# Optimization experiments

Hardware: AMD Instinct MI355X
Metric: run time of the kernel (lower is better)

## Reference

```python
import jax, jax.numpy as jnp
import numpy as np

B, S, D = 4, 2048, 1024
E, H, TOP_K = 8, 4096, 2


def setup_inputs() -> dict:
    key = jax.random.key(0)
    ks = jax.random.split(key, 5)
    scale = 0.02
    return {
        "x": jax.random.normal(ks[0], (B, S, D), dtype=jnp.float32),
        "Wr": jax.random.normal(ks[1], (D, E), dtype=jnp.float32) * scale,
        "br": jnp.zeros((E,), dtype=jnp.float32),
        "W1": jax.random.normal(ks[2], (E, D, H), dtype=jnp.float32) * scale,
        "b1": jnp.zeros((E, H), dtype=jnp.float32),
        "W2": jax.random.normal(ks[3], (E, H, D), dtype=jnp.float32) * scale,
        "b2": jnp.zeros((E, D), dtype=jnp.float32),
    }


def reference(x, Wr, br, W1, b1, W2, b2):
    b, s, d = x.shape
    xf = x.reshape(-1, d)                                   # [T, D]
    gate = jax.nn.softmax(xf @ Wr + br, axis=-1)            # [T, E]
    top_w, top_i = jax.lax.top_k(gate, TOP_K)               # [T, K]
    top_w = top_w / jnp.sum(top_w, axis=-1, keepdims=True)
    # combine[t, e] = sum_i top_w[t, i] * 1{top_i[t, i] == e}
    combine = jnp.sum(jax.nn.one_hot(top_i, E, dtype=xf.dtype) * top_w[..., None], axis=1)  # [T, E]
    # Dense all-expert FFN (same math as the masked per-expert loops in torch)
    h = jax.nn.gelu(jnp.einsum('td,edh->teh', xf, W1) + b1, approximate=False)  # [T, E, H]
    out = jnp.einsum('teh,ehd,te->td', h, W2, combine) + combine @ b2           # [T, D]
    return out.reshape(b, s, d)
```

## Files before the change

kernel.cpp:

```cpp
#include <hip/hip_runtime.h>
#include <cstdio>


#define T_TOK 8192
#define DIM   1024
#define NEXP  8
#define HID   4096
#define MAXR  17408

typedef float          f32x4   __attribute__((ext_vector_type(4)));
typedef short          bf16x8  __attribute__((ext_vector_type(8)));
typedef unsigned short u16x8   __attribute__((ext_vector_type(8)));
typedef unsigned short u16x4   __attribute__((ext_vector_type(4)));

static __device__ __forceinline__ unsigned short f2bf(float f) {
  unsigned int u = __builtin_bit_cast(unsigned int, f);
  u = (u + 0x7FFFu + ((u >> 16) & 1u)) >> 16;
  return (unsigned short)u;
}

static __device__ __forceinline__ void gl16(const void* g, void* l) {
  __builtin_amdgcn_global_load_lds(
      (const __attribute__((address_space(1))) unsigned int*)g,
      (__attribute__((address_space(3))) unsigned int*)l,
      16, 0, 0);
}

__global__ __launch_bounds__(256) void router_k(const float* __restrict__ x,
                                                const float* __restrict__ Wr,
                                                const float* __restrict__ br,
                                                int* __restrict__ meta,
                                                int2* __restrict__ top_i,
                                                float2* __restrict__ top_w) {
  int lane = threadIdx.x & 63;
  int wid  = threadIdx.x >> 6;
  int t = blockIdx.x * 4 + wid;
  const float* xp = x + (size_t)t * DIM + lane * 16;
  float acc[NEXP];
#pragma unroll
  for (int e = 0; e < NEXP; ++e) acc[e] = 0.f;
#pragma unroll
  for (int j = 0; j < 16; j += 4) {
    float4 xv = *(const float4*)(xp + j);
    const float* wp = Wr + (size_t)(lane * 16 + j) * NEXP;
#pragma unroll
    for (int jj = 0; jj < 4; ++jj) {
      float xs = jj == 0 ? xv.x : jj == 1 ? xv.y : jj == 2 ? xv.z : xv.w;
      float4 w0 = *(const float4*)(wp + jj * NEXP);
      float4 w1 = *(const float4*)(wp + jj * NEXP + 4);
      acc[0] += xs * w0.x; acc[1] += xs * w0.y; acc[2] += xs * w0.z; acc[3] += xs * w0.w;
      acc[4] += xs * w1.x; acc[5] += xs * w1.y; acc[6] += xs * w1.z; acc[7] += xs * w1.w;
    }
  }
#pragma unroll
  for (int off = 32; off > 0; off >>= 1) {
#pragma unroll
    for (int e = 0; e < NEXP; ++e) acc[e] += __shfl_xor(acc[e], off);
  }
  if (lane == 0) {
    float l[NEXP];
#pragma unroll
    for (int e = 0; e < NEXP; ++e) l[e] = acc[e] + br[e];
    int e1 = 0;
#pragma unroll
    for (int e = 1; e < NEXP; ++e) if (l[e] > l[e1]) e1 = e;
    int e2 = (e1 == 0) ? 1 : 0;
#pragma unroll
    for (int e = 0; e < NEXP; ++e) if (e != e1 && l[e] > l[e2]) e2 = e;
    float g  = expf(l[e2] - l[e1]);
    float w1 = 1.f / (1.f + g);
    top_i[t] = make_int2(e1, e2);
    top_w[t] = make_float2(w1, 1.f - w1);
    atomicAdd(&meta[e1], 1);
    atomicAdd(&meta[e2], 1);
  }
}

__global__ void prefix_k(int* __restrict__ meta) {
  if (threadIdx.x == 0) {
    int s = 0;
#pragma unroll
    for (int e = 0; e < NEXP; ++e) {
      meta[16 + e] = s;
      s += (meta[e] + 127) & ~127;
    }
    meta[24] = s;
    meta[25] = s;
  }
}

__global__ __launch_bounds__(256) void fill_k(int* __restrict__ tok_of_row,
                                              float* __restrict__ wt_of_row) {
  int i = blockIdx.x * 256 + threadIdx.x;
  if (i < MAXR) { tok_of_row[i] = 0; wt_of_row[i] = 0.f; }
}

__global__ __launch_bounds__(256) void scatter_k(const int2* __restrict__ top_i,
                                                 const float2* __restrict__ top_w,
                                                 int* __restrict__ meta,
                                                 int* __restrict__ row_of,
                                                 int* __restrict__ tok_of_row,
                                                 float* __restrict__ wt_of_row) {
  int t = blockIdx.x * 256 + threadIdx.x;
  int2  ei = top_i[t];
  float2 w = top_w[t];
  int p = atomicAdd(&meta[8 + ei.x], 1);
  int r = meta[16 + ei.x] + p;
  tok_of_row[r] = t; wt_of_row[r] = w.x; row_of[t * 2] = r;
  p = atomicAdd(&meta[8 + ei.y], 1);
  r = meta[16 + ei.y] + p;
  tok_of_row[r] = t; wt_of_row[r] = w.y; row_of[t * 2 + 1] = r;
}

__global__ __launch_bounds__(256) void gather_k(const float* __restrict__ x,
                                                const int* __restrict__ tok_of_row,
                                                const int* __restrict__ meta,
                                                unsigned short* __restrict__ xg) {
  int r = blockIdx.x;
  if (r >= meta[25]) return;
  int t = tok_of_row[r];
  int c = threadIdx.x * 4;
  float4 v = *(const float4*)(x + (size_t)t * DIM + c);
  u16x4 o;
  o[0] = f2bf(v.x); o[1] = f2bf(v.y); o[2] = f2bf(v.z); o[3] = f2bf(v.w);
  *(u16x4*)(xg + (size_t)r * DIM + c) = o;
}

__global__ __launch_bounds__(256) void transpose_convert_k(const float* __restrict__ W,
                                                           unsigned short* __restrict__ WT,
                                                           int R, int C) {
  __shared__ float tile[32][33];
  int e = blockIdx.z;
  int c0 = blockIdx.x * 32, r0 = blockIdx.y * 32;
  const float* Wp = W + (size_t)e * R * C;
  unsigned short* Op = WT + (size_t)e * R * C;
  int tr = threadIdx.x >> 3;
  int tc = (threadIdx.x & 7) * 4;
  float4 v = *(const float4*)(Wp + (size_t)(r0 + tr) * C + c0 + tc);
  tile[tr][tc] = v.x; tile[tr][tc + 1] = v.y; tile[tr][tc + 2] = v.z; tile[tr][tc + 3] = v.w;
  __syncthreads();
  int oc  = threadIdx.x >> 3;
  int orr = (threadIdx.x & 7) * 4;
  u16x4 o;
#pragma unroll
  for (int j = 0; j < 4; ++j) o[j] = f2bf(tile[orr + j][oc]);
  *(u16x4*)(Op + (size_t)(c0 + oc) * R + r0 + orr) = o;
}

template <int KTOT, int NTOT, int EPI>
__global__ __launch_bounds__(256) void gemm_k(const unsigned short* __restrict__ A,
                                              const unsigned short* __restrict__ Bt,
                                              const float* __restrict__ bias,
                                              const int* __restrict__ meta,
                                              const float* __restrict__ wt_of_row,
                                              void* __restrict__ Cout) {
  constexpr int NXB = MAXR / 128;
  constexpr int NWG = NXB * (NTOT / 128);
  int id = (blockIdx.x & 7) * (NWG / 8) + (blockIdx.x >> 3);
  int row0 = (id % NXB) * 128;
  int n0   = (id / NXB) * 128;
  if (row0 >= meta[25]) return;
  int e = 0;
  while (meta[17 + e] <= row0) ++e;
  const unsigned short* Bp = Bt + (size_t)e * NTOT * KTOT;

  __shared__ __align__(16) unsigned short Ash[128 * 32];
  __shared__ __align__(16) unsigned short Bsh[128 * 32];

  int tid = threadIdx.x;
  int lane = tid & 63, wid = tid >> 6;
  int wm = wid >> 1, wn = wid & 1;
  int rs = tid >> 2;
  int cs = (tid & 3) * 8;

  const unsigned short* Ag = A  + (size_t)(row0 + rs) * KTOT + cs;
  const unsigned short* Bg = Bp + (size_t)(n0   + rs) * KTOT + cs;
  unsigned short* Al = Ash + tid * 8;
  unsigned short* Bl = Bsh + tid * 8;

  f32x4 acc[4][4];
#pragma unroll
  for (int i = 0; i < 4; ++i)
#pragma unroll
    for (int j = 0; j < 4; ++j) acc[i][j] = (f32x4){0.f, 0.f, 0.f, 0.f};

  int am = lane & 15, ak = (lane >> 4) * 8;

  for (int kt = 0; kt < KTOT; kt += 32) {
    __syncthreads();
    gl16(Ag + kt, Al);
    gl16(Ag + 64 * KTOT + kt, Al + 2048);
    gl16(Bg + kt, Bl);
    gl16(Bg + 64 * KTOT + kt, Bl + 2048);
    __syncthreads();
    bf16x8 af[4], bfr[4];
#pragma unroll
    for (int i = 0; i < 4; ++i)
      af[i] = *(const bf16x8*)(Ash + (wm * 64 + i * 16 + am) * 32 + ak);
#pragma unroll
    for (int j = 0; j < 4; ++j)
      bfr[j] = *(const bf16x8*)(Bsh + (wn * 64 + j * 16 + am) * 32 + ak);
#pragma unroll
    for (int i = 0; i < 4; ++i)
#pragma unroll
      for (int j = 0; j < 4; ++j)
        acc[i][j] = __builtin_amdgcn_mfma_f32_16x16x32_bf16(af[i], bfr[j], acc[i][j], 0, 0, 0);
  }

  int rbase = row0 + wm * 64 + (lane >> 4) * 4;
  int nbase = n0 + wn * 64 + (lane & 15);
  if constexpr (EPI == 0) {
    unsigned short* Hp = (unsigned short*)Cout;
    const float* bp = bias + (size_t)e * NTOT;
#pragma unroll
    for (int i = 0; i < 4; ++i) {
#pragma unroll
      for (int j = 0; j < 4; ++j) {
        int n = nbase + j * 16;
        float bv = bp[n];
#pragma unroll
        for (int rg = 0; rg < 4; ++rg) {
          int m = rbase + i * 16 + rg;
          float v = acc[i][j][rg] + bv;
          v = 0.5f * v * (1.f + erff(v * 0.70710678118654752f));
          Hp[(size_t)m * NTOT + n] = f2bf(v);
        }
      }
    }
  } else {
    float* Yp = (float*)Cout;
    const float* bp = bias + (size_t)e * NTOT;
#pragma unroll
    for (int i = 0; i < 4; ++i) {
#pragma unroll
      for (int rg = 0; rg < 4; ++rg) {
        int m = rbase + i * 16 + rg;
        float wt = wt_of_row[m];
#pragma unroll
        for (int j = 0; j < 4; ++j) {
          int n = nbase + j * 16;
          Yp[(size_t)m * NTOT + n] = (acc[i][j][rg] + bp[n]) * wt;
        }
      }
    }
  }
}

__global__ __launch_bounds__(256) void combine_k(const float* __restrict__ y,
                                                 const int* __restrict__ row_of,
                                                 float* __restrict__ out) {
  int t = blockIdx.x;
  int r0 = row_of[t * 2], r1 = row_of[t * 2 + 1];
  int c = threadIdx.x * 4;
  float4 a = *(const float4*)(y + (size_t)r0 * DIM + c);
  float4 b = *(const float4*)(y + (size_t)r1 * DIM + c);
  *(float4*)(out + (size_t)t * DIM + c) =
      make_float4(a.x + b.x, a.y + b.y, a.z + b.z, a.w + b.w);
}

extern "C" void kernel_launch(void* const* d_in, const int* in_sizes, int n_in,
                              void* d_out, int out_size, void* d_ws, size_t ws_size,
                              hipStream_t stream) {
  const float* x  = (const float*)d_in[0];
  const float* Wr = (const float*)d_in[1];
  const float* br = (const float*)d_in[2];
  const float* W1 = (const float*)d_in[3];
  const float* b1 = (const float*)d_in[4];
  const float* W2 = (const float*)d_in[5];
  const float* b2 = (const float*)d_in[6];
  float* out = (float*)d_out;

  char* base = (char*)d_ws;
  size_t off = 0;
  auto carve = [&](size_t bytes) -> void* {
    void* r = base + off;
    off = (off + bytes + 255) & ~(size_t)255;
    return r;
  };
  int*            meta       = (int*)carve(26 * 4);
  int2*           top_i      = (int2*)carve((size_t)T_TOK * 8);
  float2*         top_w      = (float2*)carve((size_t)T_TOK * 8);
  int*            row_of     = (int*)carve((size_t)T_TOK * 2 * 4);
  int*            tok_of_row = (int*)carve((size_t)MAXR * 4);
  float*          wt_of_row  = (float*)carve((size_t)MAXR * 4);
  unsigned short* xg         = (unsigned short*)carve((size_t)MAXR * DIM * 2);
  unsigned short* W1bT       = (unsigned short*)carve((size_t)NEXP * DIM * HID * 2);
  unsigned short* W2bT       = (unsigned short*)carve((size_t)NEXP * DIM * HID * 2);
  unsigned short* hbuf       = (unsigned short*)carve((size_t)MAXR * HID * 2);
  float*          ybuf       = (float*)carve((size_t)MAXR * DIM * 4);
  if (off > ws_size) {
    fprintf(stderr, "kernel_launch: ws_size too small: need %zu have %zu\n", off, ws_size);
    return;
  }

  hipMemsetAsync(meta, 0, 26 * 4, stream);
  hipLaunchKernelGGL(transpose_convert_k, dim3(HID / 32, DIM / 32, NEXP), dim3(256), 0, stream,
                     W1, W1bT, DIM, HID);
  hipLaunchKernelGGL(transpose_convert_k, dim3(DIM / 32, HID / 32, NEXP), dim3(256), 0, stream,
                     W2, W2bT, HID, DIM);
  hipLaunchKernelGGL(fill_k, dim3((MAXR + 255) / 256), dim3(256), 0, stream,
                     tok_of_row, wt_of_row);
  hipLaunchKernelGGL(router_k, dim3(T_TOK / 4), dim3(256), 0, stream,
                     x, Wr, br, meta, top_i, top_w);
  hipLaunchKernelGGL(prefix_k, dim3(1), dim3(64), 0, stream, meta);
  hipLaunchKernelGGL(scatter_k, dim3(T_TOK / 256), dim3(256), 0, stream,
                     top_i, top_w, meta, row_of, tok_of_row, wt_of_row);
  hipLaunchKernelGGL(gather_k, dim3(MAXR), dim3(256), 0, stream, x, tok_of_row, meta, xg);
  hipLaunchKernelGGL((gemm_k<DIM, HID, 0>), dim3(MAXR / 128 * (HID / 128)), dim3(256), 0, stream,
                     xg, W1bT, b1, meta, wt_of_row, (void*)hbuf);
  hipLaunchKernelGGL((gemm_k<HID, DIM, 1>), dim3(MAXR / 128 * (DIM / 128)), dim3(256), 0, stream,
                     hbuf, W2bT, b2, meta, wt_of_row, (void*)ybuf);
  hipLaunchKernelGGL(combine_k, dim3(T_TOK), dim3(256), 0, stream, ybuf, row_of, out);
}
```

Measured before the change: 893.7 us.

## Use 256x256 double-buffered swizzled GEMM tiles and atomic scatter-combine into output

Replaces the 128x128 single-buffered GEMM with a 512-thread 256x256 tile kernel. It double-buffers LDS in K-halves with interleaved barrier phases and an XOR swizzle to avoid bank conflicts, and raises MFMA priority with setprio. Expert row padding grows to 256 to match the larger tiles. The second GEMM now atomically adds weighted results straight into the zeroed output, which removes the ybuf round trip and the combine kernel. The cost is larger padding waste, float atomics to global memory, and 128 KB of LDS per workgroup.

Result: slower. 952.5 us (+6.6%).

```diff
diff --git a/kernel.cpp b/kernel.cpp
--- a/kernel.cpp
+++ b/kernel.cpp
@@ -6,11 +6,10 @@
 #define DIM   1024
 #define NEXP  8
 #define HID   4096
-#define MAXR  17408
+#define MAXR  18432
 
 typedef float          f32x4   __attribute__((ext_vector_type(4)));
 typedef short          bf16x8  __attribute__((ext_vector_type(8)));
-typedef unsigned short u16x8   __attribute__((ext_vector_type(8)));
 typedef unsigned short u16x4   __attribute__((ext_vector_type(4)));
 
 static __device__ __forceinline__ unsigned short f2bf(float f) {
@@ -25,6 +24,8 @@
       (__attribute__((address_space(3))) unsigned int*)l,
       16, 0, 0);
 }
+
+#define FENCE() asm volatile("" ::: "memory")
 
 __global__ __launch_bounds__(256) void router_k(const float* __restrict__ x,
                                                 const float* __restrict__ Wr,
@@ -82,7 +83,7 @@
 #pragma unroll
     for (int e = 0; e < NEXP; ++e) {
       meta[16 + e] = s;
-      s += (meta[e] + 127) & ~127;
+      s += (meta[e] + 255) & ~255;
     }
     meta[24] = s;
     meta[25] = s;
@@ -147,115 +148,150 @@
   *(u16x4*)(Op + (size_t)(c0 + oc) * R + r0 + orr) = o;
 }
 
+
+template <int KH, int MH>
+__device__ __forceinline__ void do_phase(const unsigned short* lds_, int buf,
+                                         int aoff, int boff, f32x4 (&acc)[8][4]) {
+  const unsigned short* Ar = lds_ + (buf * 4 + KH) * 8192 + aoff + MH * 2048;
+  const unsigned short* Br = lds_ + (buf * 4 + 2 + KH) * 8192 + boff;
+  bf16x8 af[4], bv[4];
+#pragma unroll
+  for (int r = 0; r < 4; ++r) af[r] = *(const bf16x8*)(Ar + r * 512);
+#pragma unroll
+  for (int n = 0; n < 4; ++n) bv[n] = *(const bf16x8*)(Br + n * 512);
+  __builtin_amdgcn_s_setprio(1);
+#pragma unroll
+  for (int r = 0; r < 4; ++r)
+#pragma unroll
+    for (int n = 0; n < 4; ++n)
+      acc[MH * 4 + r][n] =
+          __builtin_amdgcn_mfma_f32_16x16x32_bf16(af[r], bv[n], acc[MH * 4 + r][n], 0, 0, 0);
+  __builtin_amdgcn_s_setprio(0);
+}
+
 template <int KTOT, int NTOT, int EPI>
-__global__ __launch_bounds__(256) void gemm_k(const unsigned short* __restrict__ A,
-                                              const unsigned short* __restrict__ Bt,
-                                              const float* __restrict__ bias,
-                                              const int* __restrict__ meta,
-                                              const float* __restrict__ wt_of_row,
-                                              void* __restrict__ Cout) {
-  constexpr int NXB = MAXR / 128;
-  constexpr int NWG = NXB * (NTOT / 128);
-  int id = (blockIdx.x & 7) * (NWG / 8) + (blockIdx.x >> 3);
-  int row0 = (id % NXB) * 128;
-  int n0   = (id / NXB) * 128;
+__global__ __launch_bounds__(512, 2) void gemm8_k(const unsigned short* __restrict__ A,
+                                                  const unsigned short* __restrict__ Bt,
+                                                  const float* __restrict__ bias,
+                                                  const int* __restrict__ meta,
+                                                  const float* __restrict__ wt_of_row,
+                                                  const int* __restrict__ tok_of_row,
+                                                  void* __restrict__ Cout) {
+  constexpr int NTILES = NTOT / 256;
+  constexpr int NWG = (MAXR / 256) * NTILES;
+  constexpr int NT = KTOT / 64;
+  __shared__ __align__(16) unsigned short lds[65536];
+
+  int id = ((int)blockIdx.x & 7) * (NWG / 8) + ((int)blockIdx.x >> 3);
+  int row0 = (id / NTILES) * 256;
+  int n0   = (id % NTILES) * 256;
   if (row0 >= meta[25]) return;
   int e = 0;
   while (meta[17 + e] <= row0) ++e;
   const unsigned short* Bp = Bt + (size_t)e * NTOT * KTOT;
 
-  __shared__ __align__(16) unsigned short Ash[128 * 32];
-  __shared__ __align__(16) unsigned short Bsh[128 * 32];
-
   int tid = threadIdx.x;
   int lane = tid & 63, wid = tid >> 6;
-  int wm = wid >> 1, wn = wid & 1;
-  int rs = tid >> 2;
-  int cs = (tid & 3) * 8;
-
-  const unsigned short* Ag = A  + (size_t)(row0 + rs) * KTOT + cs;
-  const unsigned short* Bg = Bp + (size_t)(n0   + rs) * KTOT + cs;
-  unsigned short* Al = Ash + tid * 8;
-  unsigned short* Bl = Bsh + tid * 8;
-
-  f32x4 acc[4][4];
-#pragma unroll
-  for (int i = 0; i < 4; ++i)
-#pragma unroll
-    for (int j = 0; j < 4; ++j) acc[i][j] = (f32x4){0.f, 0.f, 0.f, 0.f};
-
-  int am = lane & 15, ak = (lane >> 4) * 8;
-
-  for (int kt = 0; kt < KTOT; kt += 32) {
-    __syncthreads();
-    gl16(Ag + kt, Al);
-    gl16(Ag + 64 * KTOT + kt, Al + 2048);
-    gl16(Bg + kt, Bl);
-    gl16(Bg + 64 * KTOT + kt, Bl + 2048);
-    __syncthreads();
-    bf16x8 af[4], bfr[4];
-#pragma unroll
-    for (int i = 0; i < 4; ++i)
-      af[i] = *(const bf16x8*)(Ash + (wm * 64 + i * 16 + am) * 32 + ak);
-#pragma unroll
-    for (int j = 0; j < 4; ++j)
-      bfr[j] = *(const bf16x8*)(Bsh + (wn * 64 + j * 16 + am) * 32 + ak);
-#pragma unroll
-    for (int i = 0; i < 4; ++i)
-#pragma unroll
-      for (int j = 0; j < 4; ++j)
-        acc[i][j] = __builtin_amdgcn_mfma_f32_16x16x32_bf16(af[i], bfr[j], acc[i][j], 0, 0, 0);
-  }
-
-  int rbase = row0 + wm * 64 + (lane >> 4) * 4;
-  int nbase = n0 + wn * 64 + (lane & 15);
+  int wm = wid >> 2, wn = wid & 3;
+
+  int r0s = tid >> 2, r1s = 128 + (tid >> 2);
+  int s0 = (tid & 3) ^ ((r0s >> 1) & 3);
+  int s1 = (tid & 3) ^ ((r1s >> 1) & 3);
+  const unsigned short* pA0 = A + (size_t)(row0 + r0s) * KTOT + s0 * 8;
+  const unsigned short* pA1 = A + (size_t)(row0 + r1s) * KTOT + s1 * 8;
+  const unsigned short* pB0 = Bp + (size_t)(n0 + r0s) * KTOT + s0 * 8;
+  const unsigned short* pB1 = Bp + (size_t)(n0 + r1s) * KTOT + s1 * 8;
+  int ldst = wid * 512;
+
+  auto stage = [&](int bufx, int mat, int kh, int kt) {
+    int rb = (bufx * 4 + mat * 2 + kh) * 8192 + ldst;
+    int ko = kt * 64 + kh * 32;
+    gl16((mat ? pB0 : pA0) + ko, (void*)(lds + rb));
+    gl16((mat ? pB1 : pA1) + ko, (void*)(lds + rb + 4096));
+  };
+
+  int sF = ((lane >> 4) ^ ((lane >> 1) & 3)) * 8;
+  int aoff = wm * 4096 + (lane & 15) * 32 + sF;
+  int boff = wn * 2048 + (lane & 15) * 32 + sF;
+
+  f32x4 acc[8][4];
+#pragma unroll
+  for (int r = 0; r < 8; ++r)
+#pragma unroll
+    for (int n = 0; n < 4; ++n) acc[r][n] = (f32x4){0.f, 0.f, 0.f, 0.f};
+
+  stage(0, 1, 0, 0); stage(0, 0, 0, 0); stage(0, 1, 1, 0); stage(0, 0, 1, 0);
+  FENCE();
+
+  for (int t = 0; t < NT - 1; ++t) {
+    int buf = t & 1, nb = buf ^ 1;
+    stage(nb, 1, 0, t + 1);
+    asm volatile("s_waitcnt vmcnt(6)" ::: "memory");
+    __builtin_amdgcn_s_barrier(); FENCE();
+    do_phase<0, 0>(lds, buf, aoff, boff, acc);
+    stage(nb, 0, 0, t + 1); FENCE();
+    __builtin_amdgcn_s_barrier(); FENCE();
+    do_phase<0, 1>(lds, buf, aoff, boff, acc);
+    stage(nb, 1, 1, t + 1);
+    asm volatile("s_waitcnt vmcnt(6)" ::: "memory");
+    __builtin_amdgcn_s_barrier(); FENCE();
+    do_phase<1, 0>(lds, buf, aoff, boff, acc);
+    stage(nb, 0, 1, t + 1); FENCE();
+    __builtin_amdgcn_s_barrier(); FENCE();
+    do_phase<1, 1>(lds, buf, aoff, boff, acc);
+  }
+  {
+    int buf = (NT - 1) & 1;
+    asm volatile("s_waitcnt vmcnt(4)" ::: "memory");
+    __builtin_amdgcn_s_barrier(); FENCE();
+    do_phase<0, 0>(lds, buf, aoff, boff, acc);
+    __builtin_amdgcn_s_barrier(); FENCE();
+    do_phase<0, 1>(lds, buf, aoff, boff, acc);
+    asm volatile("s_waitcnt vmcnt(0)" ::: "memory");
+    __builtin_amdgcn_s_barrier(); FENCE();
+    do_phase<1, 0>(lds, buf, aoff, boff, acc);
+    __builtin_amdgcn_s_barrier(); FENCE();
+    do_phase<1, 1>(lds, buf, aoff, boff, acc);
+  }
+
+  int rb2 = row0 + wm * 128 + ((lane >> 4) << 2);
+  int nb2 = n0 + wn * 64 + (lane & 15);
   if constexpr (EPI == 0) {
     unsigned short* Hp = (unsigned short*)Cout;
     const float* bp = bias + (size_t)e * NTOT;
 #pragma unroll
-    for (int i = 0; i < 4; ++i) {
-#pragma unroll
-      for (int j = 0; j < 4; ++j) {
-        int n = nbase + j * 16;
-        float bv = bp[n];
-#pragma unroll
-        for (int rg = 0; rg < 4; ++rg) {
-          int m = rbase + i * 16 + rg;
-          float v = acc[i][j][rg] + bv;
+    for (int r = 0; r < 8; ++r)
+#pragma unroll
+      for (int n = 0; n < 4; ++n) {
+        int ncol = nb2 + n * 16;
+        float bv = bp[ncol];
+#pragma unroll
+        for (int g = 0; g < 4; ++g) {
+          int m = rb2 + r * 16 + g;
+          float v = acc[r][n][g] + bv;
           v = 0.5f * v * (1.f + erff(v * 0.70710678118654752f));
-          Hp[(size_t)m * NTOT + n] = f2bf(v);
+          Hp[(size_t)m * NTOT + ncol] = f2bf(v);
         }
       }
-    }
   } else {
-    float* Yp = (float*)Cout;
+    float* Op = (float*)Cout;
     const float* bp = bias + (size_t)e * NTOT;
 #pragma unroll
-    for (int i = 0; i < 4; ++i) {
-#pragma unroll
-      for (int rg = 0; rg < 4; ++rg) {
-        int m = rbase + i * 16 + rg;
+    for (int r = 0; r < 8; ++r)
+#pragma unroll
+      for (int g = 0; g < 4; ++g) {
+        int m = rb2 + r * 16 + g;
         float wt = wt_of_row[m];
-#pragma unroll
-        for (int j = 0; j < 4; ++j) {
-          int n = nbase + j * 16;
-          Yp[(size_t)m * NTOT + n] = (acc[i][j][rg] + bp[n]) * wt;
+        if (wt != 0.f) {
+          float* orow = Op + (size_t)tok_of_row[m] * DIM;
+#pragma unroll
+          for (int n = 0; n < 4; ++n) {
+            int ncol = nb2 + n * 16;
+            atomicAdd(orow + ncol, (acc[r][n][g] + bp[ncol]) * wt);
+          }
         }
       }
-    }
-  }
-}
-
-__global__ __launch_bounds__(256) void combine_k(const float* __restrict__ y,
-                                                 const int* __restrict__ row_of,
-                                                 float* __restrict__ out) {
-  int t = blockIdx.x;
-  int r0 = row_of[t * 2], r1 = row_of[t * 2 + 1];
-  int c = threadIdx.x * 4;
-  float4 a = *(const float4*)(y + (size_t)r0 * DIM + c);
-  float4 b = *(const float4*)(y + (size_t)r1 * DIM + c);
-  *(float4*)(out + (size_t)t * DIM + c) =
-      make_float4(a.x + b.x, a.y + b.y, a.z + b.z, a.w + b.w);
+  }
 }
 
 extern "C" void kernel_launch(void* const* d_in, const int* in_sizes, int n_in,
@@ -287,13 +323,13 @@
   unsigned short* W1bT       = (unsigned short*)carve((size_t)NEXP * DIM * HID * 2);
   unsigned short* W2bT       = (unsigned short*)carve((size_t)NEXP * DIM * HID * 2);
   unsigned short* hbuf       = (unsigned short*)carve((size_t)MAXR * HID * 2);
-  float*          ybuf       = (float*)carve((size_t)MAXR * DIM * 4);
   if (off > ws_size) {
     fprintf(stderr, "kernel_launch: ws_size too small: need %zu have %zu\n", off, ws_size);
     return;
   }
 
   hipMemsetAsync(meta, 0, 26 * 4, stream);
+  hipMemsetAsync(out, 0, (size_t)out_size * 4, stream);
   hipLaunchKernelGGL(transpose_convert_k, dim3(HID / 32, DIM / 32, NEXP), dim3(256), 0, stream,
                      W1, W1bT, DIM, HID);
   hipLaunchKernelGGL(transpose_convert_k, dim3(DIM / 32, HID / 32, NEXP), dim3(256), 0, stream,
@@ -306,9 +342,8 @@
   hipLaunchKernelGGL(scatter_k, dim3(T_TOK / 256), dim3(256), 0, stream,
                      top_i, top_w, meta, row_of, tok_of_row, wt_of_row);
   hipLaunchKernelGGL(gather_k, dim3(MAXR), dim3(256), 0, stream, x, tok_of_row, meta, xg);
-  hipLaunchKernelGGL((gemm_k<DIM, HID, 0>), dim3(MAXR / 128 * (HID / 128)), dim3(256), 0, stream,
-                     xg, W1bT, b1, meta, wt_of_row, (void*)hbuf);
-  hipLaunchKernelGGL((gemm_k<HID, DIM, 1>), dim3(MAXR / 128 * (DIM / 128)), dim3(256), 0, stream,
-                     hbuf, W2bT, b2, meta, wt_of_row, (void*)ybuf);
-  hipLaunchKernelGGL(combine_k, dim3(T_TOK), dim3(256), 0, stream, ybuf, row_of, out);
-}
+  hipLaunchKernelGGL((gemm8_k<DIM, HID, 0>), dim3((MAXR / 256) * (HID / 256)), dim3(512), 0,
+                     stream, xg, W1bT, b1, meta, wt_of_row, tok_of_row, (void*)hbuf);
+  hipLaunchKernelGGL((gemm8_k<HID, DIM, 1>), dim3((MAXR / 256) * (DIM / 256)), dim3(512), 0,
+                     stream, hbuf, W2bT, b2, meta, wt_of_row, tok_of_row, (void*)out);
+}
```

## Triple-buffer GEMM LDS with swizzle and fuse combine via atomic scatter-add

Applied to the files above, without the earlier changes.

Replaces the single-buffered GEMM main loop with a three-stage LDS ring that issues async global-to-LDS loads one tile ahead, using vmcnt waits and raw barriers. An XOR swizzle on the LDS layout is meant to avoid bank conflicts, and s_setprio is raised around the MFMA block. The second GEMM now atomically adds weighted results straight into the zeroed output, which removes the fp32 y buffer and the combine kernel at the cost of float atomics and extra memset traffic. Row padding grows to 256 per expert and MAXR is enlarged to match, which adds some wasted padded rows.

Result: slower. 924.9 us (+3.5%).

```diff
diff --git a/kernel.cpp b/kernel.cpp
--- a/kernel.cpp
+++ b/kernel.cpp
@@ -6,11 +6,10 @@
 #define DIM   1024
 #define NEXP  8
 #define HID   4096
-#define MAXR  17408
+#define MAXR  18432
 
 typedef float          f32x4   __attribute__((ext_vector_type(4)));
 typedef short          bf16x8  __attribute__((ext_vector_type(8)));
-typedef unsigned short u16x8   __attribute__((ext_vector_type(8)));
 typedef unsigned short u16x4   __attribute__((ext_vector_type(4)));
 
 static __device__ __forceinline__ unsigned short f2bf(float f) {
@@ -25,6 +24,8 @@
       (__attribute__((address_space(3))) unsigned int*)l,
       16, 0, 0);
 }
+
+#define FENCE() asm volatile("" ::: "memory")
 
 __global__ __launch_bounds__(256) void router_k(const float* __restrict__ x,
                                                 const float* __restrict__ Wr,
@@ -82,7 +83,7 @@
 #pragma unroll
     for (int e = 0; e < NEXP; ++e) {
       meta[16 + e] = s;
-      s += (meta[e] + 127) & ~127;
+      s += (meta[e] + 255) & ~255;
     }
     meta[24] = s;
     meta[25] = s;
@@ -147,16 +148,56 @@
   *(u16x4*)(Op + (size_t)(c0 + oc) * R + r0 + orr) = o;
 }
 
+
+template <int CUR, bool STG, bool LAST>
+__device__ __forceinline__ void ktile(unsigned short* lds, int ko,
+                                      const unsigned short* pA0, const unsigned short* pA1,
+                                      const unsigned short* pB0, const unsigned short* pB1,
+                                      int stL, int aoff, int boff, f32x4 (&acc)[4][4]) {
+  constexpr int NXT = (CUR + 1) % 3;
+  if constexpr (STG) {
+    gl16(pA0 + ko, lds + NXT * 8192 + stL);
+    gl16(pA1 + ko, lds + NXT * 8192 + stL + 2048);
+    gl16(pB0 + ko, lds + NXT * 8192 + 4096 + stL);
+    gl16(pB1 + ko, lds + NXT * 8192 + 4096 + stL + 2048);
+    asm volatile("s_waitcnt vmcnt(4)" ::: "memory");
+  } else {
+    asm volatile("s_waitcnt vmcnt(0)" ::: "memory");
+  }
+  __builtin_amdgcn_s_barrier();
+  FENCE();
+  bf16x8 af[4], bv[4];
+#pragma unroll
+  for (int i = 0; i < 4; ++i)
+    af[i] = *(const bf16x8*)(lds + CUR * 8192 + aoff + i * 512);
+#pragma unroll
+  for (int j = 0; j < 4; ++j)
+    bv[j] = *(const bf16x8*)(lds + CUR * 8192 + boff + j * 512);
+  __builtin_amdgcn_s_setprio(1);
+#pragma unroll
+  for (int i = 0; i < 4; ++i)
+#pragma unroll
+    for (int j = 0; j < 4; ++j)
+      acc[i][j] = __builtin_amdgcn_mfma_f32_16x16x32_bf16(af[i], bv[j], acc[i][j], 0, 0, 0);
+  __builtin_amdgcn_s_setprio(0);
+  (void)ko;
+}
+
 template <int KTOT, int NTOT, int EPI>
-__global__ __launch_bounds__(256) void gemm_k(const unsigned short* __restrict__ A,
-                                              const unsigned short* __restrict__ Bt,
-                                              const float* __restrict__ bias,
-                                              const int* __restrict__ meta,
-                                              const float* __restrict__ wt_of_row,
-                                              void* __restrict__ Cout) {
+__global__ __launch_bounds__(256, 3) void gemm3_k(const unsigned short* __restrict__ A,
+                                                  const unsigned short* __restrict__ Bt,
+                                                  const float* __restrict__ bias,
+                                                  const int* __restrict__ meta,
+                                                  const float* __restrict__ wt_of_row,
+                                                  const int* __restrict__ tok_of_row,
+                                                  void* __restrict__ Cout) {
   constexpr int NXB = MAXR / 128;
   constexpr int NWG = NXB * (NTOT / 128);
-  int id = (blockIdx.x & 7) * (NWG / 8) + (blockIdx.x >> 3);
+  constexpr int NKT = KTOT / 32;
+  static_assert(NKT % 3 == 2, "tail handling assumes NKT % 3 == 2");
+  __shared__ __align__(16) unsigned short lds[24576];
+
+  int id = ((int)blockIdx.x & 7) * (NWG / 8) + ((int)blockIdx.x >> 3);
   int row0 = (id % NXB) * 128;
   int n0   = (id / NXB) * 128;
   if (row0 >= meta[25]) return;
@@ -164,19 +205,21 @@
   while (meta[17 + e] <= row0) ++e;
   const unsigned short* Bp = Bt + (size_t)e * NTOT * KTOT;
 
-  __shared__ __align__(16) unsigned short Ash[128 * 32];
-  __shared__ __align__(16) unsigned short Bsh[128 * 32];
-
   int tid = threadIdx.x;
   int lane = tid & 63, wid = tid >> 6;
   int wm = wid >> 1, wn = wid & 1;
-  int rs = tid >> 2;
-  int cs = (tid & 3) * 8;
-
-  const unsigned short* Ag = A  + (size_t)(row0 + rs) * KTOT + cs;
-  const unsigned short* Bg = Bp + (size_t)(n0   + rs) * KTOT + cs;
-  unsigned short* Al = Ash + tid * 8;
-  unsigned short* Bl = Bsh + tid * 8;
+
+  int s = (tid & 3) ^ ((tid >> 3) & 3);
+  const unsigned short* pA0 = A + (size_t)(row0 + (tid >> 2)) * KTOT + s * 8;
+  const unsigned short* pA1 = pA0 + (size_t)64 * KTOT;
+  const unsigned short* pB0 = Bp + (size_t)(n0 + (tid >> 2)) * KTOT + s * 8;
+  const unsigned short* pB1 = pB0 + (size_t)64 * KTOT;
+  int stL = wid * 512;
+
+  int am = lane & 15;
+  int sF = ((lane >> 4) ^ ((lane >> 1) & 3)) * 8;
+  int aoff = (wm * 64 + am) * 32 + sF;
+  int boff = 4096 + (wn * 64 + am) * 32 + sF;
 
   f32x4 acc[4][4];
 #pragma unroll
@@ -184,78 +227,56 @@
 #pragma unroll
     for (int j = 0; j < 4; ++j) acc[i][j] = (f32x4){0.f, 0.f, 0.f, 0.f};
 
-  int am = lane & 15, ak = (lane >> 4) * 8;
-
-  for (int kt = 0; kt < KTOT; kt += 32) {
-    __syncthreads();
-    gl16(Ag + kt, Al);
-    gl16(Ag + 64 * KTOT + kt, Al + 2048);
-    gl16(Bg + kt, Bl);
-    gl16(Bg + 64 * KTOT + kt, Bl + 2048);
-    __syncthreads();
-    bf16x8 af[4], bfr[4];
-#pragma unroll
-    for (int i = 0; i < 4; ++i)
-      af[i] = *(const bf16x8*)(Ash + (wm * 64 + i * 16 + am) * 32 + ak);
-#pragma unroll
-    for (int j = 0; j < 4; ++j)
-      bfr[j] = *(const bf16x8*)(Bsh + (wn * 64 + j * 16 + am) * 32 + ak);
-#pragma unroll
-    for (int i = 0; i < 4; ++i)
-#pragma unroll
-      for (int j = 0; j < 4; ++j)
-        acc[i][j] = __builtin_amdgcn_mfma_f32_16x16x32_bf16(af[i], bfr[j], acc[i][j], 0, 0, 0);
-  }
-
-  int rbase = row0 + wm * 64 + (lane >> 4) * 4;
-  int nbase = n0 + wn * 64 + (lane & 15);
+  gl16(pA0, lds + stL);          gl16(pA1, lds + stL + 2048);
+  gl16(pB0, lds + 4096 + stL);   gl16(pB1, lds + 4096 + stL + 2048);
+  FENCE();
+
+  for (int t = 0; t < NKT - 2; t += 3) {
+    ktile<0, true, false>(lds, (t + 1) * 32, pA0, pA1, pB0, pB1, stL, aoff, boff, acc);
+    ktile<1, true, false>(lds, (t + 2) * 32, pA0, pA1, pB0, pB1, stL, aoff, boff, acc);
+    ktile<2, true, false>(lds, (t + 3) * 32, pA0, pA1, pB0, pB1, stL, aoff, boff, acc);
+  }
+  ktile<0, true, false>(lds, (NKT - 1) * 32, pA0, pA1, pB0, pB1, stL, aoff, boff, acc);
+  ktile<1, false, true>(lds, 0, pA0, pA1, pB0, pB1, stL, aoff, boff, acc);
+
+  int rbase = row0 + wm * 64 + ((lane >> 4) << 2);
+  int nbase = n0 + wn * 64 + am;
   if constexpr (EPI == 0) {
     unsigned short* Hp = (unsigned short*)Cout;
     const float* bp = bias + (size_t)e * NTOT;
 #pragma unroll
-    for (int i = 0; i < 4; ++i) {
+    for (int i = 0; i < 4; ++i)
 #pragma unroll
       for (int j = 0; j < 4; ++j) {
         int n = nbase + j * 16;
         float bv = bp[n];
 #pragma unroll
-        for (int rg = 0; rg < 4; ++rg) {
-          int m = rbase + i * 16 + rg;
-          float v = acc[i][j][rg] + bv;
+        for (int g = 0; g < 4; ++g) {
+          int m = rbase + i * 16 + g;
+          float v = acc[i][j][g] + bv;
           v = 0.5f * v * (1.f + erff(v * 0.70710678118654752f));
           Hp[(size_t)m * NTOT + n] = f2bf(v);
         }
       }
-    }
   } else {
-    float* Yp = (float*)Cout;
+    float* Op = (float*)Cout;
     const float* bp = bias + (size_t)e * NTOT;
 #pragma unroll
-    for (int i = 0; i < 4; ++i) {
-#pragma unroll
-      for (int rg = 0; rg < 4; ++rg) {
-        int m = rbase + i * 16 + rg;
+    for (int i = 0; i < 4; ++i)
+#pragma unroll
+      for (int g = 0; g < 4; ++g) {
+        int m = rbase + i * 16 + g;
         float wt = wt_of_row[m];
-#pragma unroll
-        for (int j = 0; j < 4; ++j) {
-          int n = nbase + j * 16;
-          Yp[(size_t)m * NTOT + n] = (acc[i][j][rg] + bp[n]) * wt;
+        if (wt != 0.f) {
+          float* orow = Op + (size_t)tok_of_row[m] * DIM;
+#pragma unroll
+          for (int j = 0; j < 4; ++j) {
+            int n = nbase + j * 16;
+            atomicAdd(orow + n, (acc[i][j][g] + bp[n]) * wt);
+          }
         }
       }
-    }
-  }
-}
-
-__global__ __launch_bounds__(256) void combine_k(const float* __restrict__ y,
-                                                 const int* __restrict__ row_of,
-                                                 float* __restrict__ out) {
-  int t = blockIdx.x;
-  int r0 = row_of[t * 2], r1 = row_of[t * 2 + 1];
-  int c = threadIdx.x * 4;
-  float4 a = *(const float4*)(y + (size_t)r0 * DIM + c);
-  float4 b = *(const float4*)(y + (size_t)r1 * DIM + c);
-  *(float4*)(out + (size_t)t * DIM + c) =
-      make_float4(a.x + b.x, a.y + b.y, a.z + b.z, a.w + b.w);
+  }
 }
 
 extern "C" void kernel_launch(void* const* d_in, const int* in_sizes, int n_in,
@@ -287,13 +308,13 @@
   unsigned short* W1bT       = (unsigned short*)carve((size_t)NEXP * DIM * HID * 2);
   unsigned short* W2bT       = (unsigned short*)carve((size_t)NEXP * DIM * HID * 2);
   unsigned short* hbuf       = (unsigned short*)carve((size_t)MAXR * HID * 2);
-  float*          ybuf       = (float*)carve((size_t)MAXR * DIM * 4);
   if (off > ws_size) {
     fprintf(stderr, "kernel_launch: ws_size too small: need %zu have %zu\n", off, ws_size);
     return;
   }
 
   hipMemsetAsync(meta, 0, 26 * 4, stream);
+  hipMemsetAsync(out, 0, (size_t)out_size * 4, stream);
   hipLaunchKernelGGL(transpose_convert_k, dim3(HID / 32, DIM / 32, NEXP), dim3(256), 0, stream,
                      W1, W1bT, DIM, HID);
   hipLaunchKernelGGL(transpose_convert_k, dim3(DIM / 32, HID / 32, NEXP), dim3(256), 0, stream,
@@ -306,9 +327,8 @@
   hipLaunchKernelGGL(scatter_k, dim3(T_TOK / 256), dim3(256), 0, stream,
                      top_i, top_w, meta, row_of, tok_of_row, wt_of_row);
   hipLaunchKernelGGL(gather_k, dim3(MAXR), dim3(256), 0, stream, x, tok_of_row, meta, xg);
-  hipLaunchKernelGGL((gemm_k<DIM, HID, 0>), dim3(MAXR / 128 * (HID / 128)), dim3(256), 0, stream,
-                     xg, W1bT, b1, meta, wt_of_row, (void*)hbuf);
-  hipLaunchKernelGGL((gemm_k<HID, DIM, 1>), dim3(MAXR / 128 * (DIM / 128)), dim3(256), 0, stream,
-                     hbuf, W2bT, b2, meta, wt_of_row, (void*)ybuf);
-  hipLaunchKernelGGL(combine_k, dim3(T_TOK), dim3(256), 0, stream, ybuf, row_of, out);
-}
+  hipLaunchKernelGGL((gemm3_k<DIM, HID, 0>), dim3((MAXR / 128) * (HID / 128)), dim3(256), 0,
+                     stream, xg, W1bT, b1, meta, wt_of_row, tok_of_row, (void*)hbuf);
+  hipLaunchKernelGGL((gemm3_k<HID, DIM, 1>), dim3((MAXR / 128) * (DIM / 128)), dim3(256), 0,
+                     stream, hbuf, W2bT, b2, meta, wt_of_row, tok_of_row, (void*)out);
+}
```
